# Kernel optimization log

Measured on AMD Instinct MI355X. Metric: run time of the kernel, lower is better.

The kernel has to match this reference:

```python
import jax, jax.numpy as jnp
import numpy as np

D_MODEL = 1024
N_HEADS = 16
D_HEAD = D_MODEL // N_HEADS
SEQ = 2048
BATCH = 2


def setup_inputs() -> dict:
    key = jax.random.key(0)
    ks = jax.random.split(key, 9)
    s = 1.0 / np.sqrt(D_MODEL)
    inp = {
        "x": jax.random.normal(ks[0], (BATCH, SEQ, D_MODEL), dtype=jnp.float32),
        "Wq": jax.random.uniform(ks[1], (D_MODEL, D_MODEL), jnp.float32, -s, s),
        "bq": jax.random.uniform(ks[2], (D_MODEL,), jnp.float32, -s, s),
        "Wk": jax.random.uniform(ks[3], (D_MODEL, D_MODEL), jnp.float32, -s, s),
        "bk": jax.random.uniform(ks[4], (D_MODEL,), jnp.float32, -s, s),
        "Wv": jax.random.uniform(ks[5], (D_MODEL, D_MODEL), jnp.float32, -s, s),
        "bv": jax.random.uniform(ks[6], (D_MODEL,), jnp.float32, -s, s),
        "Wo": jax.random.uniform(ks[7], (D_MODEL, D_MODEL), jnp.float32, -s, s),
        "bo": jax.random.uniform(ks[8], (D_MODEL,), jnp.float32, -s, s),
    }
    return inp


def reference(x, Wq, bq, Wk, bk, Wv, bv, Wo, bo):
    B, S, D = x.shape
    H, Dh = N_HEADS, D_HEAD
    # QKV projections (nn.Linear: x @ W.T + b; here W stored as [in, out])
    q = (x @ Wq + bq).reshape(B, S, H, Dh).transpose(0, 2, 1, 3)  # [B,H,S,Dh]
    k = (x @ Wk + bk).reshape(B, S, H, Dh).transpose(0, 2, 1, 3)
    v = (x @ Wv + bv).reshape(B, S, H, Dh).transpose(0, 2, 1, 3)
    scores = jnp.einsum("bhqd,bhkd->bhqk", q, k) / jnp.sqrt(jnp.float32(Dh))
    causal = jnp.tril(jnp.ones((S, S), dtype=bool))  # [S,S]
    scores = jnp.where(causal[None, None], scores, jnp.float32(-jnp.inf))
    attn = jax.nn.softmax(scores, axis=-1)
    # dropout is identity in eval mode
    h = jnp.einsum("bhqk,bhkd->bhqd", attn, v)  # [B,H,S,Dh]
    h = h.transpose(0, 2, 1, 3).reshape(B, S, D)
    return h @ Wo + bo
```

## Files before the change

### kernel.cpp

```cpp
#include <hip/hip_runtime.h>

typedef unsigned short u16;
typedef unsigned int u32;
typedef __attribute__((ext_vector_type(8))) __bf16 bf16x8;
typedef __attribute__((ext_vector_type(4))) float f32x4;
typedef __attribute__((ext_vector_type(4))) unsigned short u16x4;
typedef __attribute__((ext_vector_type(2))) unsigned int u32x2;

#define SEQ 2048
#define DM 1024
#define NH 16
#define DH 64

__device__ __forceinline__ float fexp2(float x) {
  return __builtin_amdgcn_exp2f(x);
}

__device__ __forceinline__ unsigned short f2bf(float f) {
  unsigned u = __builtin_bit_cast(unsigned, f);
  u += 0x7fffu + ((u >> 16) & 1u);
  return (unsigned short)(u >> 16);
}

__device__ __forceinline__ u32 cvtpk(float lo, float hi) {
  u32 r;
  asm("v_cvt_pk_bf16_f32 %0, %1, %2" : "=v"(r) : "v"(lo), "v"(hi));
  return r;
}

__device__ __forceinline__ void gload_lds16(const u16* g, u16* l) {
  __builtin_amdgcn_global_load_lds(
      (const __attribute__((address_space(1))) u16*)g,
      (__attribute__((address_space(3))) u16*)l, 16, 0, 0);
}

__global__ __launch_bounds__(256) void cvt_kernel(const float* __restrict__ in,
                                                  u16* __restrict__ out, int n4) {
  int id = blockIdx.x * 256 + threadIdx.x;
  if (id >= n4) return;
  float4 v = ((const float4*)in)[id];
  u16x4 o = { f2bf(v.x), f2bf(v.y), f2bf(v.z), f2bf(v.w) };
  ((u16x4*)out)[id] = o;
}

__global__ __launch_bounds__(256) void wtrans_kernel(const float* __restrict__ W0,
                                                     const float* __restrict__ W1,
                                                     const float* __restrict__ W2,
                                                     const float* __restrict__ W3,
                                                     u16* __restrict__ WtBase) {
  const float* W = (blockIdx.z == 0) ? W0 : (blockIdx.z == 1) ? W1
                 : (blockIdx.z == 2) ? W2 : W3;
  u16* Wt = WtBase + ((size_t)blockIdx.z << 20);
  __shared__ float tile[32][33];
  int tx = threadIdx.x & 31, ty = threadIdx.x >> 5;
  int k0 = blockIdx.y * 32, n0 = blockIdx.x * 32;
#pragma unroll
  for (int j = 0; j < 32; j += 8)
    tile[ty + j][tx] = W[(size_t)(k0 + ty + j) * DM + n0 + tx];
  __syncthreads();
#pragma unroll
  for (int j = 0; j < 32; j += 8)
    Wt[(size_t)(n0 + ty + j) * DM + k0 + tx] = f2bf(tile[tx][ty + j]);
}

template <int BM, int BN>
__global__ __launch_bounds__(256) void gemm_kernel(
    const u16* __restrict__ A, const u16* __restrict__ WtBase,
    const float* __restrict__ b0, const float* __restrict__ b1,
    const float* __restrict__ b2,
    void* __restrict__ O0, void* __restrict__ O1, void* __restrict__ O2,
    int modeBase) {
  constexpr int MR = BM / 32, NR = BN / 32;
  const int Kd = 1024, Nd = 1024;
  const int mode = modeBase + blockIdx.z;
  const u16* Bt = WtBase + ((size_t)blockIdx.z << 20);
  const float* bias = (blockIdx.z == 0) ? b0 : (blockIdx.z == 1) ? b1 : b2;
  void* Out = (blockIdx.z == 0) ? O0 : (blockIdx.z == 1) ? O1 : O2;

  __shared__ u16 As[2][BM * 32];
  __shared__ u16 Bs[2][BN * 32];
  const int tid = threadIdx.x;
  const int lane = tid & 63, w = tid >> 6;
  const int lrow = lane & 15, u = lane >> 4;
  const int wr = w >> 1, wc = w & 1;
  const int brow = blockIdx.y * BM, bcol = blockIdx.x * BN;

  f32x4 acc[MR][NR] = {};

  const int srow = tid >> 2;
  const int scol = (tid & 3) * 8;
  const u16* aP = A + (size_t)(brow + srow) * Kd + scol;
  const u16* bP = Bt + (size_t)(bcol + srow) * Kd + scol;

  auto stage = [&](int kt, int buf) {
#pragma unroll
    for (int i = 0; i < BM / 64; ++i)
      gload_lds16(aP + (size_t)i * 64 * Kd + kt, As[buf] + i * 2048 + w * 512);
#pragma unroll
    for (int i = 0; i < BN / 64; ++i)
      gload_lds16(bP + (size_t)i * 64 * Kd + kt, Bs[buf] + i * 2048 + w * 512);
  };

  stage(0, 0);
  __syncthreads();

  for (int it = 0; it < 32; ++it) {
    const int cur = it & 1;
    if (it + 1 < 32) stage((it + 1) * 32, cur ^ 1);
    bf16x8 af[MR], bfr[NR];
#pragma unroll
    for (int m = 0; m < MR; ++m)
      af[m] = *(const bf16x8*)(As[cur] + (wr * (BM / 2) + m * 16 + lrow) * 32 + u * 8);
#pragma unroll
    for (int n = 0; n < NR; ++n)
      bfr[n] = *(const bf16x8*)(Bs[cur] + (wc * (BN / 2) + n * 16 + lrow) * 32 + u * 8);
#pragma unroll
    for (int m = 0; m < MR; ++m)
#pragma unroll
      for (int n = 0; n < NR; ++n)
        acc[m][n] = __builtin_amdgcn_mfma_f32_16x16x32_bf16(af[m], bfr[n], acc[m][n], 0, 0, 0);
    __syncthreads();
  }

  const int r0 = brow + wr * (BM / 2) + u * 4;
  const int c0 = bcol + wc * (BN / 2) + lrow;
#pragma unroll
  for (int m = 0; m < MR; ++m) {
#pragma unroll
    for (int n = 0; n < NR; ++n) {
      const int col = c0 + n * 16;
      const float bv = bias[col];
      if (mode == 3) {
        float* O = (float*)Out;
#pragma unroll
        for (int i = 0; i < 4; ++i) {
          int row = r0 + m * 16 + i;
          O[(size_t)row * Nd + col] = acc[m][n][i] + bv;
        }
      } else if (mode == 2) {
        const int rowb = r0 + m * 16;
        const int b = rowb >> 11, s = rowb & 2047;
        const int h = col >> 6, dh = col & 63;
        u16x4 pk;
#pragma unroll
        for (int i = 0; i < 4; ++i) pk[i] = f2bf(acc[m][n][i] + bv);
        u16* O = (u16*)Out;
        *(u16x4*)(O + ((size_t)((b * NH + h) * DH + dh) * SEQ + s)) = pk;
      } else {
        const float sc = (mode == 0) ? 0.1803368801111204f : 1.0f;
        u16* O = (u16*)Out;
#pragma unroll
        for (int i = 0; i < 4; ++i) {
          int row = r0 + m * 16 + i;
          int b = row >> 11, s = row & 2047;
          int h = col >> 6, dh = col & 63;
          O[((size_t)(b * NH + h) * SEQ + s) * DH + dh] = f2bf((acc[m][n][i] + bv) * sc);
        }
      }
    }
  }
}

__device__ __forceinline__ void softmax_update(f32x4 (&s)[4], f32x4 (&hacc)[4],
                                               float& m_i, float& l_i) {
  float pg0 = fmaxf(fmaxf(s[0][0], s[0][1]), fmaxf(s[0][2], s[0][3]));
  float pg1 = fmaxf(fmaxf(s[1][0], s[1][1]), fmaxf(s[1][2], s[1][3]));
  float pg2 = fmaxf(fmaxf(s[2][0], s[2][1]), fmaxf(s[2][2], s[2][3]));
  float pg3 = fmaxf(fmaxf(s[3][0], s[3][1]), fmaxf(s[3][2], s[3][3]));
  float pmax = fmaxf(fmaxf(pg0, pg1), fmaxf(pg2, pg3));
  pmax = fmaxf(pmax, __shfl_xor(pmax, 16));
  pmax = fmaxf(pmax, __shfl_xor(pmax, 32));
  if (__any(pmax > m_i + 8.0f)) {
    const float mnew = fmaxf(m_i, pmax);
    const float scl = fexp2(m_i - mnew);
    l_i *= scl;
#pragma unroll
    for (int g = 0; g < 4; ++g) hacc[g] *= scl;
    m_i = mnew;
  }
  float rs = 0.f;
#pragma unroll
  for (int g = 0; g < 4; ++g)
#pragma unroll
    for (int i = 0; i < 4; ++i) {
      const float p = fexp2(s[g][i] - m_i);
      s[g][i] = p;
      rs += p;
    }
  rs += __shfl_xor(rs, 16);
  rs += __shfl_xor(rs, 32);
  l_i += rs;
}

__device__ __forceinline__ void write_p(u16* ps, const f32x4 (&s)[4], int lrow, int u) {
#pragma unroll
  for (int g = 0; g < 4; ++g) {
    u32x2 pw = { cvtpk(s[g][0], s[g][1]), cvtpk(s[g][2], s[g][3]) };
    *(u32x2*)(ps + ((lrow * 128 + ((g * 32 + u * 8) ^ ((lrow & 7) << 4))) >> 1)) = pw;
  }
}

__global__ __launch_bounds__(256, 2) void attn_kernel(const u16* __restrict__ Qb,
                                                      const u16* __restrict__ Kb,
                                                      const u16* __restrict__ Vt,
                                                      u16* __restrict__ Hh) {
  const int px = blockIdx.x, bh = blockIdx.y;
  const int qtA = px, qtB = 31 - px;
  const int tid = threadIdx.x, lane = tid & 63, w = tid >> 6;
  const int lrow = lane & 15, u = lane >> 4;

  const u16* Qp = Qb + (size_t)bh * SEQ * DH;
  const u16* Kp = Kb + (size_t)bh * SEQ * DH;
  const u16* Vp = Vt + (size_t)bh * DH * SEQ;

  __shared__ u16 KV[2][2][4096];
  __shared__ u16 Ps[4][2][1024];

  const int q0A = qtA * 64 + w * 16, q0B = qtB * 64 + w * 16;
  bf16x8 qfA[2], qfB[2];
#pragma unroll
  for (int ks = 0; ks < 2; ++ks) {
    qfA[ks] = *(const bf16x8*)(Qp + (size_t)(q0A + lrow) * DH + ks * 32 + u * 8);
    qfB[ks] = *(const bf16x8*)(Qp + (size_t)(q0B + lrow) * DH + ks * 32 + u * 8);
  }

  float mA = -1e30f, lA = 0.f, mB = -1e30f, lB = 0.f;
  f32x4 haccA[4], haccB[4];
#pragma unroll
  for (int g = 0; g < 4; ++g) {
    haccA[g] = (f32x4){0.f, 0.f, 0.f, 0.f};
    haccB[g] = (f32x4){0.f, 0.f, 0.f, 0.f};
  }

  auto stage = [&](int kt, int buf) {
#pragma unroll
    for (int i = 0; i < 2; ++i) {
      const int p = i * 4096 + tid * 16;
      const int row = p >> 7;
      const int c16 = ((p >> 4) & 7) ^ (row & 7);
      gload_lds16(Kp + (size_t)(kt * 64 + row) * 64 + c16 * 8, &KV[buf][0][p >> 1]);
      gload_lds16(Vp + (size_t)row * 2048 + (size_t)kt * 64 + c16 * 8, &KV[buf][1][p >> 1]);
    }
  };

  stage(0, 0);
  __syncthreads();

  const int wq = w * 16 + lrow;
  const int nkt = qtB + 1;
  for (int kt = 0; kt < nkt; ++kt) {
    const int cur = kt & 1;
    if (kt + 1 < nkt) stage(kt + 1, cur ^ 1);
    const u16* bufK = KV[cur][0];
    const u16* bufV = KV[cur][1];
    const bool doA = (kt <= qtA);

    bf16x8 kf[2][4];
#pragma unroll
    for (int ks = 0; ks < 2; ++ks) {
      const int c = ks * 64 + u * 16;
#pragma unroll
      for (int g = 0; g < 4; ++g) {
        const int r = g * 16 + lrow;
        kf[ks][g] = *(const bf16x8*)(bufK + ((r * 128 + (c ^ ((r & 7) << 4))) >> 1));
      }
    }
    f32x4 sA[4] = {}, sB[4] = {};
#pragma unroll
    for (int ks = 0; ks < 2; ++ks)
#pragma unroll
      for (int g = 0; g < 4; ++g)
        sB[g] = __builtin_amdgcn_mfma_f32_16x16x32_bf16(kf[ks][g], qfB[ks], sB[g], 0, 0, 0);
    if (doA) {
#pragma unroll
      for (int ks = 0; ks < 2; ++ks)
#pragma unroll
        for (int g = 0; g < 4; ++g)
          sA[g] = __builtin_amdgcn_mfma_f32_16x16x32_bf16(kf[ks][g], qfA[ks], sA[g], 0, 0, 0);
    }
    if (kt == qtB) {
#pragma unroll
      for (int g = 0; g < 4; ++g) {
        const int kb = g * 16 + u * 4;
#pragma unroll
        for (int i = 0; i < 4; ++i)
          if (kb + i > wq) sB[g][i] = -1e30f;
      }
    }
    softmax_update(sB, haccB, mB, lB);
    write_p(&Ps[w][1][0], sB, lrow, u);
    if (doA) {
      if (kt == qtA) {
#pragma unroll
        for (int g = 0; g < 4; ++g) {
          const int kb = g * 16 + u * 4;
#pragma unroll
          for (int i = 0; i < 4; ++i)
            if (kb + i > wq) sA[g][i] = -1e30f;
        }
      }
      softmax_update(sA, haccA, mA, lA);
      write_p(&Ps[w][0][0], sA, lrow, u);
    }
    bf16x8 vf[2][4], pfB[2], pfA[2];
#pragma unroll
    for (int ks = 0; ks < 2; ++ks) {
      const int c = ks * 64 + u * 16;
#pragma unroll
      for (int g = 0; g < 4; ++g) {
        const int r = g * 16 + lrow;
        vf[ks][g] = *(const bf16x8*)(bufV + ((r * 128 + (c ^ ((r & 7) << 4))) >> 1));
      }
      pfB[ks] = *(const bf16x8*)(&Ps[w][1][0] + ((lrow * 128 + (c ^ ((lrow & 7) << 4))) >> 1));
      if (doA)
        pfA[ks] = *(const bf16x8*)(&Ps[w][0][0] + ((lrow * 128 + (c ^ ((lrow & 7) << 4))) >> 1));
    }
#pragma unroll
    for (int ks = 0; ks < 2; ++ks)
#pragma unroll
      for (int g = 0; g < 4; ++g)
        haccB[g] = __builtin_amdgcn_mfma_f32_16x16x32_bf16(vf[ks][g], pfB[ks], haccB[g], 0, 0, 0);
    if (doA) {
#pragma unroll
      for (int ks = 0; ks < 2; ++ks)
#pragma unroll
        for (int g = 0; g < 4; ++g)
          haccA[g] = __builtin_amdgcn_mfma_f32_16x16x32_bf16(vf[ks][g], pfA[ks], haccA[g], 0, 0, 0);
    }
    __syncthreads();
  }

  const int b = bh >> 4, h = bh & 15;
  {
    const float inv = 1.0f / lA;
    u16* dst = Hh + ((size_t)b * SEQ + (q0A + lrow)) * DM + h * DH + u * 4;
#pragma unroll
    for (int g = 0; g < 4; ++g) {
      u32x2 pk = { cvtpk(haccA[g][0] * inv, haccA[g][1] * inv),
                   cvtpk(haccA[g][2] * inv, haccA[g][3] * inv) };
      *(u32x2*)(dst + g * 16) = pk;
    }
  }
  {
    const float inv = 1.0f / lB;
    u16* dst = Hh + ((size_t)b * SEQ + (q0B + lrow)) * DM + h * DH + u * 4;
#pragma unroll
    for (int g = 0; g < 4; ++g) {
      u32x2 pk = { cvtpk(haccB[g][0] * inv, haccB[g][1] * inv),
                   cvtpk(haccB[g][2] * inv, haccB[g][3] * inv) };
      *(u32x2*)(dst + g * 16) = pk;
    }
  }
}

extern "C" void kernel_launch(void* const* d_in, const int* in_sizes, int n_in,
                              void* d_out, int out_size, void* d_ws, size_t ws_size,
                              hipStream_t stream) {
  const float* x  = (const float*)d_in[0];
  const float* Wq = (const float*)d_in[1];
  const float* bq = (const float*)d_in[2];
  const float* Wk = (const float*)d_in[3];
  const float* bk = (const float*)d_in[4];
  const float* Wv = (const float*)d_in[5];
  const float* bv = (const float*)d_in[6];
  const float* Wo = (const float*)d_in[7];
  const float* bo = (const float*)d_in[8];
  float* out = (float*)d_out;

  char* ws = (char*)d_ws;
  u16* Xb  = (u16*)(ws);
  u16* Wt  = (u16*)(ws + (8u << 20));
  u16* Qb  = (u16*)(ws + (16u << 20));
  u16* Kb  = (u16*)(ws + (24u << 20));
  u16* Vt  = (u16*)(ws + (32u << 20));
  u16* Hh  = (u16*)(ws + (40u << 20));
  (void)in_sizes; (void)n_in; (void)out_size; (void)ws_size;

  cvt_kernel<<<4096, 256, 0, stream>>>(x, Xb, 4096 * 1024 / 4);
  dim3 tg(32, 32, 4);
  wtrans_kernel<<<tg, 256, 0, stream>>>(Wq, Wk, Wv, Wo, Wt);
  dim3 gq(16, 32, 3);
  gemm_kernel<128, 64><<<gq, 256, 0, stream>>>(Xb, Wt, bq, bk, bv, Qb, Kb, Vt, 0);
  dim3 ga(16, 32);
  attn_kernel<<<ga, 256, 0, stream>>>(Qb, Kb, Vt, Hh);
  dim3 go(16, 64, 1);
  gemm_kernel<64, 64><<<go, 256, 0, stream>>>(Hh, Wt + (3u << 20), bo, bo, bo, out, out, out, 3);
}
```

Measured before the change: 214.0 us.

## Deepen GEMM K-tile to 64 with XOR-swizzled LDS and larger block tiles

Each GEMM stage now loads a K-slice of 64 instead of 32, halving the number of loop iterations and barriers. The LDS layout uses an XOR swizzle on 16-byte chunks to avoid bank conflicts when reading MFMA fragments. Block tiles grow to 128x128 for the QKV projection and 128x64 for the output projection, raising data reuse per block at the cost of more LDS, more registers and fewer blocks.

```diff
diff --git a/kernel.cpp b/kernel.cpp
--- a/kernel.cpp
+++ b/kernel.cpp
@@ -77,8 +77,8 @@
   const float* bias = (blockIdx.z == 0) ? b0 : (blockIdx.z == 1) ? b1 : b2;
   void* Out = (blockIdx.z == 0) ? O0 : (blockIdx.z == 1) ? O1 : O2;
 
-  __shared__ u16 As[2][BM * 32];
-  __shared__ u16 Bs[2][BN * 32];
+  __shared__ u16 As[2][BM * 64];
+  __shared__ u16 Bs[2][BN * 64];
   const int tid = threadIdx.x;
   const int lane = tid & 63, w = tid >> 6;
   const int lrow = lane & 15, u = lane >> 4;
@@ -87,38 +87,49 @@
 
   f32x4 acc[MR][NR] = {};
 
-  const int srow = tid >> 2;
-  const int scol = (tid & 3) * 8;
-  const u16* aP = A + (size_t)(brow + srow) * Kd + scol;
-  const u16* bP = Bt + (size_t)(bcol + srow) * Kd + scol;
-
   auto stage = [&](int kt, int buf) {
 #pragma unroll
-    for (int i = 0; i < BM / 64; ++i)
-      gload_lds16(aP + (size_t)i * 64 * Kd + kt, As[buf] + i * 2048 + w * 512);
-#pragma unroll
-    for (int i = 0; i < BN / 64; ++i)
-      gload_lds16(bP + (size_t)i * 64 * Kd + kt, Bs[buf] + i * 2048 + w * 512);
+    for (int i = 0; i < BM / 32; ++i) {
+      const int p = i * 4096 + tid * 16;
+      const int row = p >> 7;
+      const int chunk = ((p >> 4) & 7) ^ (row & 7);
+      gload_lds16(A + (size_t)(brow + row) * Kd + kt + chunk * 8, As[buf] + (p >> 1));
+    }
+#pragma unroll
+    for (int i = 0; i < BN / 32; ++i) {
+      const int p = i * 4096 + tid * 16;
+      const int row = p >> 7;
+      const int chunk = ((p >> 4) & 7) ^ (row & 7);
+      gload_lds16(Bt + (size_t)(bcol + row) * Kd + kt + chunk * 8, Bs[buf] + (p >> 1));
+    }
   };
 
   stage(0, 0);
   __syncthreads();
 
-  for (int it = 0; it < 32; ++it) {
+  for (int it = 0; it < 16; ++it) {
     const int cur = it & 1;
-    if (it + 1 < 32) stage((it + 1) * 32, cur ^ 1);
-    bf16x8 af[MR], bfr[NR];
-#pragma unroll
-    for (int m = 0; m < MR; ++m)
-      af[m] = *(const bf16x8*)(As[cur] + (wr * (BM / 2) + m * 16 + lrow) * 32 + u * 8);
-#pragma unroll
-    for (int n = 0; n < NR; ++n)
-      bfr[n] = *(const bf16x8*)(Bs[cur] + (wc * (BN / 2) + n * 16 + lrow) * 32 + u * 8);
-#pragma unroll
-    for (int m = 0; m < MR; ++m)
-#pragma unroll
-      for (int n = 0; n < NR; ++n)
-        acc[m][n] = __builtin_amdgcn_mfma_f32_16x16x32_bf16(af[m], bfr[n], acc[m][n], 0, 0, 0);
+    if (it + 1 < 16) stage((it + 1) * 64, cur ^ 1);
+#pragma unroll
+    for (int ks = 0; ks < 2; ++ks) {
+      const int c = ks * 64 + u * 16;
+      bf16x8 af[MR], bfr[NR];
+#pragma unroll
+      for (int m = 0; m < MR; ++m) {
+        const int r = wr * (BM / 2) + m * 16 + lrow;
+        af[m] = *(const bf16x8*)(As[cur] + ((r * 128 + (c ^ ((r & 7) << 4))) >> 1));
+      }
+#pragma unroll
+      for (int n = 0; n < NR; ++n) {
+        const int r = wc * (BN / 2) + n * 16 + lrow;
+        bfr[n] = *(const bf16x8*)(Bs[cur] + ((r * 128 + (c ^ ((r & 7) << 4))) >> 1));
+      }
+#pragma unroll
+      for (int m = 0; m < MR; ++m)
+#pragma unroll
+        for (int n = 0; n < NR; ++n)
+          acc[m][n] = __builtin_amdgcn_mfma_f32_16x16x32_bf16(af[m], bfr[n], acc[m][n], 0, 0, 0);
+    }
     __syncthreads();
   }
 
@@ -379,10 +390,10 @@
   cvt_kernel<<<4096, 256, 0, stream>>>(x, Xb, 4096 * 1024 / 4);
   dim3 tg(32, 32, 4);
   wtrans_kernel<<<tg, 256, 0, stream>>>(Wq, Wk, Wv, Wo, Wt);
-  dim3 gq(16, 32, 3);
-  gemm_kernel<128, 64><<<gq, 256, 0, stream>>>(Xb, Wt, bq, bk, bv, Qb, Kb, Vt, 0);
+  dim3 gq(8, 32, 3);
+  gemm_kernel<128, 128><<<gq, 256, 0, stream>>>(Xb, Wt, bq, bk, bv, Qb, Kb, Vt, 0);
   dim3 ga(16, 32);
   attn_kernel<<<ga, 256, 0, stream>>>(Qb, Kb, Vt, Hh);
-  dim3 go(16, 64, 1);
-  gemm_kernel<64, 64><<<go, 256, 0, stream>>>(Hh, Wt + (3u << 20), bo, bo, bo, out, out, out, 3);
-}
+  dim3 go(16, 32, 1);
+  gemm_kernel<128, 64><<<go, 256, 0, stream>>>(Hh, Wt + (3u << 20), bo, bo, bo, out, out, out, 3);
+}
```

New measurement: 207.6 us. 1.03x faster.
